# Kernel optimization log

Hardware: AMD Instinct MI355X
Metric: run time of the kernel (lower is better)

## Reference

```python
import jax, jax.numpy as jnp
import numpy as np

B, C, H, W = 2, 256, 64, 64  # C = in_channels; x has 2*C channels
DQ = C // 16


def setup_inputs() -> dict:
    key = jax.random.key(0)
    ks = jax.random.split(key, 10)
    s = 0.05
    return {
        "x": jax.random.normal(ks[0], (B, 2 * C, H, W), dtype=jnp.float32),
        "Wq": jax.random.normal(ks[1], (DQ, C), dtype=jnp.float32) * s,
        "bq": jax.random.normal(ks[2], (DQ,), dtype=jnp.float32) * s,
        "Wk": jax.random.normal(ks[3], (DQ, C), dtype=jnp.float32) * s,
        "bk": jax.random.normal(ks[4], (DQ,), dtype=jnp.float32) * s,
        "Wv": jax.random.normal(ks[5], (C, C), dtype=jnp.float32) * s,
        "bv": jax.random.normal(ks[6], (C,), dtype=jnp.float32) * s,
        "Wpt": jax.random.normal(ks[7], (C, 2 * C), dtype=jnp.float32) * s,
        "bpt": jax.random.normal(ks[8], (C,), dtype=jnp.float32) * s,
        "gamma": jnp.full((1,), 0.5, dtype=jnp.float32),  # original inits to 0; nonzero for a non-trivial output
    }


def _conv1x1(x, Wt, b):
    # 1x1 conv == per-pixel linear map over channels
    return jnp.einsum("bchw,dc->bdhw", x, Wt) + b[None, :, None, None]


def reference(x, Wq, bq, Wk, bk, Wv, bv, Wpt, bpt, gamma):
    n = x.shape[1] // 2
    x1, x2 = x[:, :n], x[:, n:]
    b, c, h, w = x1.shape
    hw = h * w

    def qkv(xi):
        q = _conv1x1(xi, Wq, bq).reshape(b, DQ, hw)   # [B,dq,HW]
        k = _conv1x1(xi, Wk, bk).reshape(b, DQ, hw)   # [B,dq,HW]
        v = _conv1x1(xi, Wv, bv).reshape(b, c, hw)    # [B,C,HW]
        return q, k, v

    q1, k1, v1 = qkv(x1)
    q2, k2, v2 = qkv(x2)

    # attn[b,i,j] = softmax_j( q[:,i] . k[:,j] )  (no scaling, as in original)
    attn1 = jax.nn.softmax(jnp.einsum("bdi,bdj->bij", q1, k1), axis=-1)  # [B,HW,HW]
    attn2 = jax.nn.softmax(jnp.einsum("bdi,bdj->bij", q2, k2), axis=-1)

    def apply_attn(v, attn):
        # out[b,c,i] = sum_j v[b,c,j] * attn[b,i,j]
        return jnp.einsum("bcj,bij->bci", v, attn).reshape(b, c, h, w)

    out11 = apply_attn(v1, attn1)
    out12 = apply_attn(v2, attn1)
    out21 = apply_attn(v1, attn2)
    out22 = apply_attn(v2, attn2)

    o1 = _conv1x1(jnp.concatenate([out11, out12], axis=1), Wpt, bpt)  # [B,C,H,W]
    o2 = _conv1x1(jnp.concatenate([out21, out22], axis=1), Wpt, bpt)

    out = gamma * jnp.concatenate([o1, o2], axis=1) + x
    return out
```

## Files before the change

### kernel.cpp

```cpp
#include <hip/hip_runtime.h>
#include <hip/hip_bf16.h>


#define HW 4096
#define CC 256
#define DQ 16

typedef __hip_bfloat16 bf16;
struct alignas(8) bh4 { bf16 x, y, z, w; };
typedef __bf16 bf16x8 __attribute__((ext_vector_type(8)));
typedef float  f32x4  __attribute__((ext_vector_type(4)));

static __device__ __forceinline__ float b2f(bf16 v) { return __bfloat162float(v); }

static __device__ __forceinline__ void load_lds16(const void* g, void* l) {
    __builtin_amdgcn_global_load_lds(
        (const __attribute__((address_space(1))) unsigned int*)g,
        (__attribute__((address_space(3))) unsigned int*)l, 16, 0, 0);
}

static __device__ __forceinline__ bf16x8 ones8() {
    union { unsigned int u[4]; bf16x8 v; } t;
    t.u[0] = t.u[1] = t.u[2] = t.u[3] = 0x3F803F80u;
    return t.v;
}

struct ConvArgs { const void* src[9]; float* dst[9]; int n[9]; };
__global__ void convert_weights(ConvArgs a, const unsigned short* __restrict__ probe) {
    int seg = blockIdx.y;
    int i = blockIdx.x * 256 + threadIdx.x;
    bool isb = probe[0] != 0;
    if (i < a.n[seg])
        a.dst[seg][i] = isb ? b2f(((const bf16*)a.src[seg])[i])
                            : ((const float*)a.src[seg])[i];
}

__global__ void w_to_bf16(const float* __restrict__ Wqf, const float* __restrict__ Wkf,
                          bf16* __restrict__ Wqb, bf16* __restrict__ Wkb) {
    int i = blockIdx.x * 256 + threadIdx.x;
    const float* s = blockIdx.y ? Wkf : Wqf;
    bf16* d = blockIdx.y ? Wkb : Wqb;
    d[i] = __float2bfloat16(s[i]);
}

__global__ void convert_x_t(const void* __restrict__ xsrc, bf16* __restrict__ Xt,
                            const unsigned short* __restrict__ probe) {
    __shared__ float T[64][65];
    int t = threadIdx.x;
    int j0 = blockIdx.x * 64, e0 = blockIdx.y * 64, b = blockIdx.z;
    bool isb = probe[0] != 0;
    int j_l = t & 63, er0 = (t >> 6) * 16;
#pragma unroll
    for (int r = 0; r < 16; ++r) {
        size_t src = ((size_t)(b * 512 + e0 + er0 + r)) * HW + j0 + j_l;
        T[er0 + r][j_l] = isb ? b2f(((const bf16*)xsrc)[src]) : ((const float*)xsrc)[src];
    }
    __syncthreads();
    int e_w = t & 63, jr0 = (t >> 6) * 16;
#pragma unroll
    for (int r = 0; r < 16; ++r)
        Xt[((size_t)b * HW + j0 + jr0 + r) * 512 + e0 + e_w] = __float2bfloat16(T[e_w][jr0 + r]);
}

__global__ void build_mc(const float* __restrict__ Wv, const float* __restrict__ bv,
                         const float* __restrict__ Wpt, const float* __restrict__ bpt,
                         bf16* __restrict__ McB, float* __restrict__ btot) {
    int blk = blockIdx.x, tid = threadIdx.x;
    if (blk < 512) {
        int d = blk >> 1;
        int c = ((blk & 1) << 8) + tid;
        int half = c >> 8, cm = c & 255;
        float acc = 0.f;
        for (int e = 0; e < 256; ++e)
            acc = fmaf(Wpt[d * 512 + half * 256 + e], Wv[e * 256 + cm], acc);
        McB[d * 512 + c] = __float2bfloat16(acc);
    } else {
        int d = tid;
        float acc = bpt[d];
        for (int e = 0; e < 256; ++e)
            acc = fmaf(Wpt[d * 512 + e] + Wpt[d * 512 + 256 + e], bv[e], acc);
        btot[d] = acc;
    }
}

__global__ void __launch_bounds__(256)
build_qk_mfma(const bf16* __restrict__ Xt,
              const bf16* __restrict__ Wqb, const float* __restrict__ bqf,
              const bf16* __restrict__ Wkb, const float* __restrict__ bkf,
              bf16* __restrict__ Qb, bf16* __restrict__ Kb) {
    int tid = threadIdx.x;
    int lane = tid & 63, wave = tid >> 6;
    int ln = lane & 15, q = lane >> 4;
    int bh = blockIdx.y;
    int b = bh >> 1, h = bh & 1;
    int j0 = blockIdx.x * 64 + wave * 16;

    bf16x8 aQ[8], aK[8];
#pragma unroll
    for (int kk = 0; kk < 8; ++kk) {
        aQ[kk] = *(const bf16x8*)&Wqb[ln * 256 + kk * 32 + q * 8];
        aK[kk] = *(const bf16x8*)&Wkb[ln * 256 + kk * 32 + q * 8];
    }
    const bf16* Xrow = Xt + ((size_t)b * HW + j0 + ln) * 512 + h * 256;
    f32x4 dQ = {0.f, 0.f, 0.f, 0.f}, dK = {0.f, 0.f, 0.f, 0.f};
#pragma unroll
    for (int kk = 0; kk < 8; ++kk) {
        bf16x8 bx = *(const bf16x8*)&Xrow[kk * 32 + q * 8];
        dQ = __builtin_amdgcn_mfma_f32_16x16x32_bf16(aQ[kk], bx, dQ, 0, 0, 0);
        dK = __builtin_amdgcn_mfma_f32_16x16x32_bf16(aK[kk], bx, dK, 0, 0, 0);
    }
    size_t rowoff = ((size_t)bh * HW + j0 + ln) * 32;
    bh4 oq, ok;
    oq.x = __float2bfloat16(dQ[0] + bqf[q * 4 + 0]);
    oq.y = __float2bfloat16(dQ[1] + bqf[q * 4 + 1]);
    oq.z = __float2bfloat16(dQ[2] + bqf[q * 4 + 2]);
    oq.w = __float2bfloat16(dQ[3] + bqf[q * 4 + 3]);
    ok.x = __float2bfloat16(dK[0] + bkf[q * 4 + 0]);
    ok.y = __float2bfloat16(dK[1] + bkf[q * 4 + 1]);
    ok.z = __float2bfloat16(dK[2] + bkf[q * 4 + 2]);
    ok.w = __float2bfloat16(dK[3] + bkf[q * 4 + 3]);
    bh4 z; z.x = z.y = z.z = z.w = __float2bfloat16(0.f);
    *(bh4*)&Qb[rowoff + q * 4] = oq;
    *(bh4*)&Qb[rowoff + 16 + q * 4] = z;
    *(bh4*)&Kb[rowoff + q * 4] = ok;
    *(bh4*)&Kb[rowoff + 16 + q * 4] = z;
}

__global__ void __launch_bounds__(256, 2)
build_u_mfma(const bf16* __restrict__ McB, const bf16* __restrict__ Xt,
             bf16* __restrict__ Ub) {
    __shared__ __align__(16) bf16 sA[64 * 64];
    __shared__ __align__(16) bf16 sB[128 * 64];
    int tid = threadIdx.x;
    int lane = tid & 63, wave = tid >> 6;
    int ln = lane & 15, q = lane >> 4;
    int wm = (wave >> 1) * 32, wn = (wave & 1) * 64;
    int j0 = blockIdx.x * 128, c0 = blockIdx.y * 64, b = blockIdx.z;
    const bf16* Xb = Xt + (size_t)b * HW * 512;
    f32x4 acc[2][4];
#pragma unroll
    for (int mi = 0; mi < 2; ++mi)
#pragma unroll
        for (int ni = 0; ni < 4; ++ni)
#pragma unroll
            for (int r = 0; r < 4; ++r) acc[mi][ni][r] = 0.f;

    for (int e0 = 0; e0 < 512; e0 += 64) {
        __syncthreads();
#pragma unroll
        for (int r = 0; r < 2; ++r) {
            int s = r * 256 + tid;
            int row = s >> 3, jc = s & 7, jg = jc ^ (row & 7);
            load_lds16(McB + (size_t)(c0 + row) * 512 + e0 + jg * 8, sA + s * 8);
        }
#pragma unroll
        for (int r = 0; r < 4; ++r) {
            int s = r * 256 + tid;
            int row = s >> 3, jc = s & 7, jg = jc ^ (row & 7);
            load_lds16(Xb + (size_t)(j0 + row) * 512 + e0 + jg * 8, sB + s * 8);
        }
        __syncthreads();
#pragma unroll
        for (int kh = 0; kh < 2; ++kh) {
            bf16x8 af[2], bfv[4];
#pragma unroll
            for (int mi = 0; mi < 2; ++mi) {
                int row = wm + mi * 16 + ln;
                int jc = (kh * 4 + q) ^ (row & 7);
                af[mi] = *(const bf16x8*)&sA[row * 64 + jc * 8];
            }
#pragma unroll
            for (int ni = 0; ni < 4; ++ni) {
                int row = wn + ni * 16 + ln;
                int jc = (kh * 4 + q) ^ (row & 7);
                bfv[ni] = *(const bf16x8*)&sB[row * 64 + jc * 8];
            }
#pragma unroll
            for (int mi = 0; mi < 2; ++mi)
#pragma unroll
                for (int ni = 0; ni < 4; ++ni)
                    acc[mi][ni] = __builtin_amdgcn_mfma_f32_16x16x32_bf16(
                        af[mi], bfv[ni], acc[mi][ni], 0, 0, 0);
        }
    }
#pragma unroll
    for (int mi = 0; mi < 2; ++mi)
#pragma unroll
        for (int r = 0; r < 4; ++r) {
            int c = c0 + wm + mi * 16 + q * 4 + r;
#pragma unroll
            for (int ni = 0; ni < 4; ++ni) {
                int j = j0 + wn + ni * 16 + ln;
                Ub[((size_t)(b * CC + c)) * HW + j] = __float2bfloat16(acc[mi][ni][r]);
            }
        }
}

__global__ void __launch_bounds__(256, 2)
flash_attn(const bf16* __restrict__ Ub, const bf16* __restrict__ Qb,
           const bf16* __restrict__ Kb, const float* __restrict__ btot,
           const void* __restrict__ xorig, const float* __restrict__ gamf,
           void* __restrict__ outv, const unsigned short* __restrict__ probe) {
    __shared__ __align__(16) bf16 sU[2][128 * 64];
    __shared__ __align__(16) bf16 sK[2][4 * 64 * 8];
    __shared__ __align__(16) bf16 sE[64 * 64];
    int tid  = threadIdx.x;
    int lane = tid & 63, wave = tid >> 6;
    int ln = lane & 15, q = lane >> 4;
    int wm = (wave & 1) * 64, wn = (wave >> 1) * 32;
    int i0 = blockIdx.x * 64, c0 = blockIdx.y * 128;
    int bh = blockIdx.z;
    int b = bh >> 1, h = bh & 1;
    const bf16* Ubb = Ub + (size_t)b * CC * HW + (size_t)c0 * HW;
    const bf16* Kbh = Kb + (size_t)bh * HW * 32;
    const bf16x8 ONE = ones8();

    bf16x8 bq = *(const bf16x8*)&Qb[((size_t)bh * HW + i0 + wave * 16 + ln) * 32 + q * 8];

    f32x4 acc[4][2], accS[2];
#pragma unroll
    for (int ni = 0; ni < 2; ++ni) {
#pragma unroll
        for (int r = 0; r < 4; ++r) accS[ni][r] = 0.f;
#pragma unroll
        for (int mi = 0; mi < 4; ++mi)
#pragma unroll
            for (int r = 0; r < 4; ++r) acc[mi][ni][r] = 0.f;
    }

    int i_loc = wave * 16 + ln;
    int wchunk0 = (q >> 1);
    int woff = (q & 1) * 4;

    auto stage_tile = [&](int tn, int bufn) {
        int j0n = tn * 64;
#pragma unroll
        for (int r = 0; r < 4; ++r) {
            int s = r * 256 + tid;
            int row = s >> 3, jc = s & 7, jg = jc ^ (row & 7);
            load_lds16(Ubb + (size_t)row * HW + j0n + jg * 8, &sU[bufn][s * 8]);
        }
        load_lds16(Kbh + ((size_t)(j0n + (tid >> 6) * 16 + (tid & 15))) * 32
                       + ((tid >> 4) & 3) * 8,
                   &sK[bufn][tid * 8]);
    };

    stage_tile(0, 0);
    asm volatile("s_waitcnt vmcnt(0)" ::: "memory");
    __builtin_amdgcn_sched_barrier(0);
    __builtin_amdgcn_s_barrier();
    __builtin_amdgcn_sched_barrier(0);

    for (int t = 0; t < 64; ++t) {
        stage_tile((t + 1) & 63, (t + 1) & 1);

        const bf16* sKc = sK[t & 1];
#pragma unroll
        for (int js = 0; js < 4; ++js) {
            bf16x8 ak = *(const bf16x8*)&sKc[(js * 64 + lane) * 8];
            f32x4 d = {0.f, 0.f, 0.f, 0.f};
            d = __builtin_amdgcn_mfma_f32_16x16x32_bf16(ak, bq, d, 0, 0, 0);
            bh4 o;
            o.x = __float2bfloat16(__expf(d[0]));
            o.y = __float2bfloat16(__expf(d[1]));
            o.z = __float2bfloat16(__expf(d[2]));
            o.w = __float2bfloat16(__expf(d[3]));
            int chunk = (js * 2 + wchunk0) ^ (i_loc & 7);
            *(bh4*)&sE[i_loc * 64 + chunk * 8 + woff] = o;
        }

        asm volatile("s_waitcnt lgkmcnt(0)" ::: "memory");
        __builtin_amdgcn_sched_barrier(0);
        __builtin_amdgcn_s_barrier();
        __builtin_amdgcn_sched_barrier(0);

        const bf16* sUc = sU[t & 1];
        __builtin_amdgcn_s_setprio(1);
#pragma unroll
        for (int kh = 0; kh < 2; ++kh) {
            bf16x8 af[4], bfv[2];
#pragma unroll
            for (int mi = 0; mi < 4; ++mi) {
                int row = wm + mi * 16 + ln;
                int jc = (kh * 4 + q) ^ (row & 7);
                af[mi] = *(const bf16x8*)&sUc[row * 64 + jc * 8];
            }
#pragma unroll
            for (int ni = 0; ni < 2; ++ni) {
                int row = wn + ni * 16 + ln;
                int jc = (kh * 4 + q) ^ (row & 7);
                bfv[ni] = *(const bf16x8*)&sE[row * 64 + jc * 8];
            }
#pragma unroll
            for (int ni = 0; ni < 2; ++ni) {
                accS[ni] = __builtin_amdgcn_mfma_f32_16x16x32_bf16(
                    ONE, bfv[ni], accS[ni], 0, 0, 0);
#pragma unroll
                for (int mi = 0; mi < 4; ++mi)
                    acc[mi][ni] = __builtin_amdgcn_mfma_f32_16x16x32_bf16(
                        af[mi], bfv[ni], acc[mi][ni], 0, 0, 0);
            }
        }
        __builtin_amdgcn_s_setprio(0);

        asm volatile("s_waitcnt vmcnt(0) lgkmcnt(0)" ::: "memory");
        __builtin_amdgcn_sched_barrier(0);
        __builtin_amdgcn_s_barrier();
        __builtin_amdgcn_sched_barrier(0);
    }

    bool isb = probe[0] != 0;
    float g = gamf[0];
    float lv[2];
#pragma unroll
    for (int ni = 0; ni < 2; ++ni)
        lv[ni] = 1.f / accS[ni][0];
#pragma unroll
    for (int mi = 0; mi < 4; ++mi)
#pragma unroll
        for (int r = 0; r < 4; ++r) {
            int c = c0 + wm + mi * 16 + q * 4 + r;
            float bt = btot[c];
            size_t rowbase = ((size_t)(b * 512 + h * 256 + c)) * HW + i0 + wn;
#pragma unroll
            for (int ni = 0; ni < 2; ++ni) {
                size_t idx = rowbase + ni * 16 + ln;
                float xres = isb ? b2f(((const bf16*)xorig)[idx]) : ((const float*)xorig)[idx];
                float o = fmaf(g, fmaf(acc[mi][ni][r], lv[ni], bt), xres);
                if (isb) ((bf16*)outv)[idx] = __float2bfloat16(o);
                else     ((float*)outv)[idx] = o;
            }
        }
}

extern "C" void kernel_launch(void* const* d_in, const int* in_sizes, int n_in,
                              void* d_out, int out_size, void* d_ws, size_t ws_size,
                              hipStream_t stream) {
    const unsigned short* probe = (const unsigned short*)d_in[9];

    char* ws = (char*)d_ws;
    size_t off = 0;
    auto alloc = [&](size_t bytes) { size_t r = off; off = (off + bytes + 255) & ~(size_t)255; return r; };
    const int wsz[9] = {DQ * 256, DQ, DQ * 256, DQ, 256 * 256, 256, 256 * 512, 256, 1};
    float* wf[9];
    for (int t = 0; t < 9; ++t) wf[t] = (float*)(ws + alloc((size_t)wsz[t] * 4));
    bf16*  Xt   = (bf16*)(ws + alloc((size_t)2 * HW * 512 * 2));
    bf16*  McB  = (bf16*)(ws + alloc(256 * 512 * 2));
    float* btot = (float*)(ws + alloc(256 * 4));
    bf16*  Wqb  = (bf16*)(ws + alloc(DQ * 256 * 2));
    bf16*  Wkb  = (bf16*)(ws + alloc(DQ * 256 * 2));
    bf16*  Qb   = (bf16*)(ws + alloc((size_t)4 * HW * 32 * 2));
    bf16*  Kb   = (bf16*)(ws + alloc((size_t)4 * HW * 32 * 2));
    bf16*  Ub   = (bf16*)(ws + alloc((size_t)2 * CC * HW * 2));

    ConvArgs ca;
    for (int t = 0; t < 9; ++t) { ca.src[t] = d_in[t + 1]; ca.dst[t] = wf[t]; ca.n[t] = wsz[t]; }
    convert_weights<<<dim3(512, 9), 256, 0, stream>>>(ca, probe);
    w_to_bf16<<<dim3(16, 2), 256, 0, stream>>>(wf[0], wf[2], Wqb, Wkb);
    convert_x_t<<<dim3(64, 8, 2), 256, 0, stream>>>(d_in[0], Xt, probe);

    build_mc<<<513, 256, 0, stream>>>(wf[4], wf[5], wf[6], wf[7], McB, btot);
    build_qk_mfma<<<dim3(64, 4), 256, 0, stream>>>(Xt, Wqb, wf[1], Wkb, wf[3], Qb, Kb);
    build_u_mfma<<<dim3(32, 4, 2), 256, 0, stream>>>(McB, Xt, Ub);

    flash_attn<<<dim3(64, 2, 4), 256, 0, stream>>>(Ub, Qb, Kb, btot, d_in[0], wf[8], d_out, probe);
}
```

Before: 209.5 us.

## Merge prep kernels into fewer launches and triple-buffer flash attention tiles

Merges the weight conversion, bf16 casts, x transpose and Mc/btot build into one kernel, and the QK and U builds into another, cutting launches from seven to three and dropping the fp32 weight copies. In flash_attn, the U and K tiles become triple-buffered and the exp tile double-buffered. This lets the second barrier per iteration go away and loads wait on a partial vmcnt. The intent is less launch and sync overhead and better overlap of global loads with MFMA work. The cost is more LDS per block, which may lower occupancy, and exact vmcnt counting that must stay correct.

Measured after the change: 249.0 us. 18.9% more time.

```diff
diff --git a/kernel.cpp b/kernel.cpp
--- a/kernel.cpp
+++ b/kernel.cpp
@@ -12,6 +12,9 @@
 typedef float  f32x4  __attribute__((ext_vector_type(4)));
 
 static __device__ __forceinline__ float b2f(bf16 v) { return __bfloat162float(v); }
+static __device__ __forceinline__ float ldf(const void* p, size_t i, bool isb) {
+    return isb ? b2f(((const bf16*)p)[i]) : ((const float*)p)[i];
+}
 
 static __device__ __forceinline__ void load_lds16(const void* g, void* l) {
     __builtin_amdgcn_global_load_lds(
@@ -25,117 +28,117 @@
     return t.v;
 }
 
-struct ConvArgs { const void* src[9]; float* dst[9]; int n[9]; };
-__global__ void convert_weights(ConvArgs a, const unsigned short* __restrict__ probe) {
-    int seg = blockIdx.y;
-    int i = blockIdx.x * 256 + threadIdx.x;
+__global__ void __launch_bounds__(256)
+prep_xt(const void* __restrict__ xsrc,
+        const void* __restrict__ Wq_r, const void* __restrict__ bq_r,
+        const void* __restrict__ Wk_r, const void* __restrict__ bk_r,
+        const void* __restrict__ Wv_r, const void* __restrict__ bv_r,
+        const void* __restrict__ Wpt_r, const void* __restrict__ bpt_r,
+        const void* __restrict__ gam_r,
+        float* __restrict__ bqf, float* __restrict__ bkf, float* __restrict__ gamf,
+        bf16* __restrict__ Wqb, bf16* __restrict__ Wkb,
+        bf16* __restrict__ McB, float* __restrict__ btot, bf16* __restrict__ Xt,
+        const unsigned short* __restrict__ probe) {
+    __shared__ float T[64][65];
+    int bx = blockIdx.x, tid = threadIdx.x;
     bool isb = probe[0] != 0;
-    if (i < a.n[seg])
-        a.dst[seg][i] = isb ? b2f(((const bf16*)a.src[seg])[i])
-                            : ((const float*)a.src[seg])[i];
-}
-
-__global__ void w_to_bf16(const float* __restrict__ Wqf, const float* __restrict__ Wkf,
-                          bf16* __restrict__ Wqb, bf16* __restrict__ Wkb) {
-    int i = blockIdx.x * 256 + threadIdx.x;
-    const float* s = blockIdx.y ? Wkf : Wqf;
-    bf16* d = blockIdx.y ? Wkb : Wqb;
-    d[i] = __float2bfloat16(s[i]);
-}
-
-__global__ void convert_x_t(const void* __restrict__ xsrc, bf16* __restrict__ Xt,
-                            const unsigned short* __restrict__ probe) {
-    __shared__ float T[64][65];
-    int t = threadIdx.x;
-    int j0 = blockIdx.x * 64, e0 = blockIdx.y * 64, b = blockIdx.z;
-    bool isb = probe[0] != 0;
-    int j_l = t & 63, er0 = (t >> 6) * 16;
-#pragma unroll
-    for (int r = 0; r < 16; ++r) {
-        size_t src = ((size_t)(b * 512 + e0 + er0 + r)) * HW + j0 + j_l;
-        T[er0 + r][j_l] = isb ? b2f(((const bf16*)xsrc)[src]) : ((const float*)xsrc)[src];
-    }
-    __syncthreads();
-    int e_w = t & 63, jr0 = (t >> 6) * 16;
-#pragma unroll
-    for (int r = 0; r < 16; ++r)
-        Xt[((size_t)b * HW + j0 + jr0 + r) * 512 + e0 + e_w] = __float2bfloat16(T[e_w][jr0 + r]);
-}
-
-__global__ void build_mc(const float* __restrict__ Wv, const float* __restrict__ bv,
-                         const float* __restrict__ Wpt, const float* __restrict__ bpt,
-                         bf16* __restrict__ McB, float* __restrict__ btot) {
-    int blk = blockIdx.x, tid = threadIdx.x;
-    if (blk < 512) {
-        int d = blk >> 1;
-        int c = ((blk & 1) << 8) + tid;
+    if (bx < 512) {
+        int d = bx >> 1;
+        int c = ((bx & 1) << 8) + tid;
         int half = c >> 8, cm = c & 255;
         float acc = 0.f;
         for (int e = 0; e < 256; ++e)
-            acc = fmaf(Wpt[d * 512 + half * 256 + e], Wv[e * 256 + cm], acc);
+            acc = fmaf(ldf(Wpt_r, (size_t)d * 512 + half * 256 + e, isb),
+                       ldf(Wv_r, (size_t)e * 256 + cm, isb), acc);
         McB[d * 512 + c] = __float2bfloat16(acc);
+    } else if (bx == 512) {
+        int d = tid;
+        float acc = ldf(bpt_r, d, isb);
+        for (int e = 0; e < 256; ++e)
+            acc = fmaf(ldf(Wpt_r, (size_t)d * 512 + e, isb) +
+                       ldf(Wpt_r, (size_t)d * 512 + 256 + e, isb),
+                       ldf(bv_r, e, isb), acc);
+        btot[d] = acc;
+    } else if (bx < 545) {
+        int id = bx - 513;
+        const void* s = id < 16 ? Wq_r : Wk_r;
+        bf16* dst = id < 16 ? Wqb : Wkb;
+        int i = (id & 15) * 256 + tid;
+        dst[i] = __float2bfloat16(ldf(s, i, isb));
+    } else if (bx == 545) {
+        if (tid < 16) bqf[tid] = ldf(bq_r, tid, isb);
+        else if (tid < 32) bkf[tid - 16] = ldf(bk_r, tid - 16, isb);
+        else if (tid == 32) gamf[0] = ldf(gam_r, 0, isb);
     } else {
-        int d = tid;
-        float acc = bpt[d];
-        for (int e = 0; e < 256; ++e)
-            acc = fmaf(Wpt[d * 512 + e] + Wpt[d * 512 + 256 + e], bv[e], acc);
-        btot[d] = acc;
-    }
-}
-
-__global__ void __launch_bounds__(256)
-build_qk_mfma(const bf16* __restrict__ Xt,
-              const bf16* __restrict__ Wqb, const float* __restrict__ bqf,
-              const bf16* __restrict__ Wkb, const float* __restrict__ bkf,
-              bf16* __restrict__ Qb, bf16* __restrict__ Kb) {
-    int tid = threadIdx.x;
-    int lane = tid & 63, wave = tid >> 6;
-    int ln = lane & 15, q = lane >> 4;
-    int bh = blockIdx.y;
-    int b = bh >> 1, h = bh & 1;
-    int j0 = blockIdx.x * 64 + wave * 16;
-
-    bf16x8 aQ[8], aK[8];
-#pragma unroll
-    for (int kk = 0; kk < 8; ++kk) {
-        aQ[kk] = *(const bf16x8*)&Wqb[ln * 256 + kk * 32 + q * 8];
-        aK[kk] = *(const bf16x8*)&Wkb[ln * 256 + kk * 32 + q * 8];
-    }
-    const bf16* Xrow = Xt + ((size_t)b * HW + j0 + ln) * 512 + h * 256;
-    f32x4 dQ = {0.f, 0.f, 0.f, 0.f}, dK = {0.f, 0.f, 0.f, 0.f};
-#pragma unroll
-    for (int kk = 0; kk < 8; ++kk) {
-        bf16x8 bx = *(const bf16x8*)&Xrow[kk * 32 + q * 8];
-        dQ = __builtin_amdgcn_mfma_f32_16x16x32_bf16(aQ[kk], bx, dQ, 0, 0, 0);
-        dK = __builtin_amdgcn_mfma_f32_16x16x32_bf16(aK[kk], bx, dK, 0, 0, 0);
-    }
-    size_t rowoff = ((size_t)bh * HW + j0 + ln) * 32;
-    bh4 oq, ok;
-    oq.x = __float2bfloat16(dQ[0] + bqf[q * 4 + 0]);
-    oq.y = __float2bfloat16(dQ[1] + bqf[q * 4 + 1]);
-    oq.z = __float2bfloat16(dQ[2] + bqf[q * 4 + 2]);
-    oq.w = __float2bfloat16(dQ[3] + bqf[q * 4 + 3]);
-    ok.x = __float2bfloat16(dK[0] + bkf[q * 4 + 0]);
-    ok.y = __float2bfloat16(dK[1] + bkf[q * 4 + 1]);
-    ok.z = __float2bfloat16(dK[2] + bkf[q * 4 + 2]);
-    ok.w = __float2bfloat16(dK[3] + bkf[q * 4 + 3]);
-    bh4 z; z.x = z.y = z.z = z.w = __float2bfloat16(0.f);
-    *(bh4*)&Qb[rowoff + q * 4] = oq;
-    *(bh4*)&Qb[rowoff + 16 + q * 4] = z;
-    *(bh4*)&Kb[rowoff + q * 4] = ok;
-    *(bh4*)&Kb[rowoff + 16 + q * 4] = z;
+        int id = bx - 546;
+        int j0 = (id & 63) * 64, e0 = ((id >> 6) & 7) * 64, b = id >> 9;
+        int j_l = tid & 63, er0 = (tid >> 6) * 16;
+#pragma unroll
+        for (int r = 0; r < 16; ++r) {
+            size_t src = ((size_t)(b * 512 + e0 + er0 + r)) * HW + j0 + j_l;
+            T[er0 + r][j_l] = ldf(xsrc, src, isb);
+        }
+        __syncthreads();
+        int e_w = tid & 63, jr0 = (tid >> 6) * 16;
+#pragma unroll
+        for (int r = 0; r < 16; ++r)
+            Xt[((size_t)b * HW + j0 + jr0 + r) * 512 + e0 + e_w] =
+                __float2bfloat16(T[e_w][jr0 + r]);
+    }
 }
 
 __global__ void __launch_bounds__(256, 2)
-build_u_mfma(const bf16* __restrict__ McB, const bf16* __restrict__ Xt,
-             bf16* __restrict__ Ub) {
+qku(const bf16* __restrict__ Xt,
+    const bf16* __restrict__ Wqb, const float* __restrict__ bqf,
+    const bf16* __restrict__ Wkb, const float* __restrict__ bkf,
+    bf16* __restrict__ Qb, bf16* __restrict__ Kb,
+    const bf16* __restrict__ McB, bf16* __restrict__ Ub) {
     __shared__ __align__(16) bf16 sA[64 * 64];
     __shared__ __align__(16) bf16 sB[128 * 64];
     int tid = threadIdx.x;
     int lane = tid & 63, wave = tid >> 6;
     int ln = lane & 15, q = lane >> 4;
+    int bx = blockIdx.x;
+
+    if (bx < 256) {
+        int bh = bx >> 6;
+        int b = bh >> 1, h = bh & 1;
+        int j0 = (bx & 63) * 64 + wave * 16;
+        bf16x8 aQ[8], aK[8];
+#pragma unroll
+        for (int kk = 0; kk < 8; ++kk) {
+            aQ[kk] = *(const bf16x8*)&Wqb[ln * 256 + kk * 32 + q * 8];
+            aK[kk] = *(const bf16x8*)&Wkb[ln * 256 + kk * 32 + q * 8];
+        }
+        const bf16* Xrow = Xt + ((size_t)b * HW + j0 + ln) * 512 + h * 256;
+        f32x4 dQ = {0.f, 0.f, 0.f, 0.f}, dK = {0.f, 0.f, 0.f, 0.f};
+#pragma unroll
+        for (int kk = 0; kk < 8; ++kk) {
+            bf16x8 bxv = *(const bf16x8*)&Xrow[kk * 32 + q * 8];
+            dQ = __builtin_amdgcn_mfma_f32_16x16x32_bf16(aQ[kk], bxv, dQ, 0, 0, 0);
+            dK = __builtin_amdgcn_mfma_f32_16x16x32_bf16(aK[kk], bxv, dK, 0, 0, 0);
+        }
+        size_t rowoff = ((size_t)bh * HW + j0 + ln) * 32;
+        bh4 oq, ok;
+        oq.x = __float2bfloat16(dQ[0] + bqf[q * 4 + 0]);
+        oq.y = __float2bfloat16(dQ[1] + bqf[q * 4 + 1]);
+        oq.z = __float2bfloat16(dQ[2] + bqf[q * 4 + 2]);
+        oq.w = __float2bfloat16(dQ[3] + bqf[q * 4 + 3]);
+        ok.x = __float2bfloat16(dK[0] + bkf[q * 4 + 0]);
+        ok.y = __float2bfloat16(dK[1] + bkf[q * 4 + 1]);
+        ok.z = __float2bfloat16(dK[2] + bkf[q * 4 + 2]);
+        ok.w = __float2bfloat16(dK[3] + bkf[q * 4 + 3]);
+        bh4 z; z.x = z.y = z.z = z.w = __float2bfloat16(0.f);
+        *(bh4*)&Qb[rowoff + q * 4] = oq;
+        *(bh4*)&Qb[rowoff + 16 + q * 4] = z;
+        *(bh4*)&Kb[rowoff + q * 4] = ok;
+        *(bh4*)&Kb[rowoff + 16 + q * 4] = z;
+        return;
+    }
+
+    int id = bx - 256;
     int wm = (wave >> 1) * 32, wn = (wave & 1) * 64;
-    int j0 = blockIdx.x * 128, c0 = blockIdx.y * 64, b = blockIdx.z;
+    int j0 = (id & 31) * 128, c0 = ((id >> 5) & 3) * 64, b = id >> 7;
     const bf16* Xb = Xt + (size_t)b * HW * 512;
     f32x4 acc[2][4];
 #pragma unroll
@@ -201,9 +204,9 @@
            const bf16* __restrict__ Kb, const float* __restrict__ btot,
            const void* __restrict__ xorig, const float* __restrict__ gamf,
            void* __restrict__ outv, const unsigned short* __restrict__ probe) {
-    __shared__ __align__(16) bf16 sU[2][128 * 64];
-    __shared__ __align__(16) bf16 sK[2][4 * 64 * 8];
-    __shared__ __align__(16) bf16 sE[64 * 64];
+    __shared__ __align__(16) bf16 sU[3][128 * 64];
+    __shared__ __align__(16) bf16 sK[3][4 * 64 * 8];
+    __shared__ __align__(16) bf16 sE[2][64 * 64];
     int tid  = threadIdx.x;
     int lane = tid & 63, wave = tid >> 6;
     int ln = lane & 15, q = lane >> 4;
@@ -232,29 +235,35 @@
     int wchunk0 = (q >> 1);
     int woff = (q & 1) * 4;
 
-    auto stage_tile = [&](int tn, int bufn) {
-        int j0n = tn * 64;
+    auto stage_u = [&](int tn, int bufn) {
 #pragma unroll
         for (int r = 0; r < 4; ++r) {
             int s = r * 256 + tid;
             int row = s >> 3, jc = s & 7, jg = jc ^ (row & 7);
-            load_lds16(Ubb + (size_t)row * HW + j0n + jg * 8, &sU[bufn][s * 8]);
-        }
-        load_lds16(Kbh + ((size_t)(j0n + (tid >> 6) * 16 + (tid & 15))) * 32
+            load_lds16(Ubb + (size_t)row * HW + tn * 64 + jg * 8, &sU[bufn][s * 8]);
+        }
+    };
+    auto stage_k = [&](int tn, int bufn) {
+        load_lds16(Kbh + ((size_t)(tn * 64 + (tid >> 6) * 16 + (tid & 15))) * 32
                        + ((tid >> 4) & 3) * 8,
                    &sK[bufn][tid * 8]);
     };
 
-    stage_tile(0, 0);
+    stage_u(0, 0);
+    stage_k(0, 0);
+    stage_k(1, 1);
     asm volatile("s_waitcnt vmcnt(0)" ::: "memory");
     __builtin_amdgcn_sched_barrier(0);
     __builtin_amdgcn_s_barrier();
     __builtin_amdgcn_sched_barrier(0);
 
+    int bu_r = 0, bu_s = 1, bk_r = 0, bk_s = 2;
     for (int t = 0; t < 64; ++t) {
-        stage_tile((t + 1) & 63, (t + 1) & 1);
-
-        const bf16* sKc = sK[t & 1];
+        stage_u((t + 1) & 63, bu_s);
+        stage_k((t + 2) & 63, bk_s);
+
+        const bf16* sKc = sK[bk_r];
+        bf16* sEc = sE[t & 1];
 #pragma unroll
         for (int js = 0; js < 4; ++js) {
             bf16x8 ak = *(const bf16x8*)&sKc[(js * 64 + lane) * 8];
@@ -266,15 +275,15 @@
             o.z = __float2bfloat16(__expf(d[2]));
             o.w = __float2bfloat16(__expf(d[3]));
             int chunk = (js * 2 + wchunk0) ^ (i_loc & 7);
-            *(bh4*)&sE[i_loc * 64 + chunk * 8 + woff] = o;
-        }
-
-        asm volatile("s_waitcnt lgkmcnt(0)" ::: "memory");
+            *(bh4*)&sEc[i_loc * 64 + chunk * 8 + woff] = o;
+        }
+
+        asm volatile("s_waitcnt vmcnt(5) lgkmcnt(0)" ::: "memory");
         __builtin_amdgcn_sched_barrier(0);
         __builtin_amdgcn_s_barrier();
         __builtin_amdgcn_sched_barrier(0);
 
-        const bf16* sUc = sU[t & 1];
+        const bf16* sUc = sU[bu_r];
         __builtin_amdgcn_s_setprio(1);
 #pragma unroll
         for (int kh = 0; kh < 2; ++kh) {
@@ -289,7 +298,7 @@
             for (int ni = 0; ni < 2; ++ni) {
                 int row = wn + ni * 16 + ln;
                 int jc = (kh * 4 + q) ^ (row & 7);
-                bfv[ni] = *(const bf16x8*)&sE[row * 64 + jc * 8];
+                bfv[ni] = *(const bf16x8*)&sEc[row * 64 + jc * 8];
             }
 #pragma unroll
             for (int ni = 0; ni < 2; ++ni) {
@@ -303,10 +312,10 @@
         }
         __builtin_amdgcn_s_setprio(0);
 
-        asm volatile("s_waitcnt vmcnt(0) lgkmcnt(0)" ::: "memory");
-        __builtin_amdgcn_sched_barrier(0);
-        __builtin_amdgcn_s_barrier();
-        __builtin_amdgcn_sched_barrier(0);
+        bu_r = bu_r == 2 ? 0 : bu_r + 1;
+        bu_s = bu_s == 2 ? 0 : bu_s + 1;
+        bk_r = bk_r == 2 ? 0 : bk_r + 1;
+        bk_s = bk_s == 2 ? 0 : bk_s + 1;
     }
 
     bool isb = probe[0] != 0;
@@ -341,9 +350,9 @@
     char* ws = (char*)d_ws;
     size_t off = 0;
     auto alloc = [&](size_t bytes) { size_t r = off; off = (off + bytes + 255) & ~(size_t)255; return r; };
-    const int wsz[9] = {DQ * 256, DQ, DQ * 256, DQ, 256 * 256, 256, 256 * 512, 256, 1};
-    float* wf[9];
-    for (int t = 0; t < 9; ++t) wf[t] = (float*)(ws + alloc((size_t)wsz[t] * 4));
+    float* bqf  = (float*)(ws + alloc(16 * 4));
+    float* bkf  = (float*)(ws + alloc(16 * 4));
+    float* gamf = (float*)(ws + alloc(4));
     bf16*  Xt   = (bf16*)(ws + alloc((size_t)2 * HW * 512 * 2));
     bf16*  McB  = (bf16*)(ws + alloc(256 * 512 * 2));
     float* btot = (float*)(ws + alloc(256 * 4));
@@ -353,15 +362,12 @@
     bf16*  Kb   = (bf16*)(ws + alloc((size_t)4 * HW * 32 * 2));
     bf16*  Ub   = (bf16*)(ws + alloc((size_t)2 * CC * HW * 2));
 
-    ConvArgs ca;
-    for (int t = 0; t < 9; ++t) { ca.src[t] = d_in[t + 1]; ca.dst[t] = wf[t]; ca.n[t] = wsz[t]; }
-    convert_weights<<<dim3(512, 9), 256, 0, stream>>>(ca, probe);
-    w_to_bf16<<<dim3(16, 2), 256, 0, stream>>>(wf[0], wf[2], Wqb, Wkb);
-    convert_x_t<<<dim3(64, 8, 2), 256, 0, stream>>>(d_in[0], Xt, probe);
-
-    build_mc<<<513, 256, 0, stream>>>(wf[4], wf[5], wf[6], wf[7], McB, btot);
-    build_qk_mfma<<<dim3(64, 4), 256, 0, stream>>>(Xt, Wqb, wf[1], Wkb, wf[3], Qb, Kb);
-    build_u_mfma<<<dim3(32, 4, 2), 256, 0, stream>>>(McB, Xt, Ub);
-
-    flash_attn<<<dim3(64, 2, 4), 256, 0, stream>>>(Ub, Qb, Kb, btot, d_in[0], wf[8], d_out, probe);
-}
+    prep_xt<<<dim3(1570), 256, 0, stream>>>(
+        d_in[0], d_in[1], d_in[2], d_in[3], d_in[4], d_in[5], d_in[6],
+        d_in[7], d_in[8], d_in[9],
+        bqf, bkf, gamf, Wqb, Wkb, McB, btot, Xt, probe);
+
+    qku<<<dim3(512), 256, 0, stream>>>(Xt, Wqb, bqf, Wkb, bkf, Qb, Kb, McB, Ub);
+
+    flash_attn<<<dim3(64, 2, 4), 256, 0, stream>>>(Ub, Qb, Kb, btot, d_in[0], gamf, d_out, probe);
+}
```
